# Kernel optimization log

Measured on AMD Instinct MI355X. Metric: run time of the kernel, lower is better.

The kernel has to match this reference:

```python
import jax, jax.numpy as jnp
import numpy as np

N = 100000
E = 1600000
C = 128
SIM_THRESH = 0.2
DEG_THRESH = 3.0


def setup_inputs() -> dict:
    key = jax.random.key(0)
    ks = jax.random.split(key, 10)
    g = 0.1  # glorot-ish scale for prompt params
    x = jax.random.normal(ks[0], (N, C), jnp.float32)
    edge_index = jax.random.randint(ks[1], (2, E), 0, N)
    prompt_sim = jax.random.normal(ks[2], (1, C), jnp.float32) * g
    prompt_degree = jax.random.normal(ks[3], (1, C), jnp.float32) * g
    prompt_other = jax.random.normal(ks[4], (1, C), jnp.float32) * g
    readout_token = jax.random.normal(ks[5], (1, 1, C), jnp.float32) * g
    in_proj_w = jax.random.normal(ks[6], (3 * C, C), jnp.float32) / np.sqrt(C)
    in_proj_b = jnp.zeros((3 * C,), jnp.float32)
    out_proj_w = jax.random.normal(ks[7], (C, C), jnp.float32) / np.sqrt(C)
    out_proj_b = jnp.zeros((C,), jnp.float32)
    return {"x": x, "prompt_sim": prompt_sim, "prompt_degree": prompt_degree,
            "prompt_other": prompt_other, "readout_token": readout_token,
            "in_proj_w": in_proj_w, "in_proj_b": in_proj_b,
            "out_proj_w": out_proj_w, "out_proj_b": out_proj_b,
            "edge_index": edge_index}


def _forward(x, prompt_sim, prompt_degree, prompt_other, readout_token,
             in_proj_w, in_proj_b, out_proj_w, out_proj_b, edge_index):
    n = x.shape[0]
    row, col = edge_index[0], edge_index[1]

    # per-edge cosine similarity, scatter-added to destination nodes
    x_norm = x / jnp.sqrt(jnp.sum(x * x, axis=1, keepdims=True))  # [N,C]
    e = jnp.sum(x_norm[row] * x_norm[col], axis=1)                # [E]
    c = jax.ops.segment_sum(e, col, num_segments=n)               # [N]
    deg = jax.ops.segment_sum(jnp.ones_like(e), col, num_segments=n)  # [N]
    csim = jax.lax.stop_gradient(c / deg)                         # nan for deg==0 -> mask False

    sim_mask = csim <= SIM_THRESH                                 # [N] bool
    deg_mask = jax.lax.stop_gradient(deg) <= DEG_THRESH
    other_mask = ~(sim_mask | deg_mask)

    neg1 = jnp.float32(-1.0)
    slot0 = jnp.where(sim_mask[:, None], prompt_sim, neg1)        # [N,C]
    slot1 = jnp.where(deg_mask[:, None], prompt_degree, neg1)
    slot2 = jnp.where(other_mask[:, None], prompt_other, neg1)
    rec = jnp.stack([slot0, slot1, slot2], axis=1)                # [N,3,C]
    ro = jnp.broadcast_to(readout_token, (n, 1, x.shape[1]))
    rec = jnp.concatenate([ro, rec], axis=1)                      # [N,4,C]

    # key_padding_mask: True where slot entirely -1 (unfilled)
    kpm = jnp.all(rec == neg1, axis=-1)                           # [N,4]

    # single-head MHA over the 4 prompt slots per node
    qkv = rec @ in_proj_w.T + in_proj_b                           # [N,4,3C]
    q, k, v = jnp.split(qkv, 3, axis=-1)
    scale = 1.0 / np.sqrt(rec.shape[-1])
    scores = jnp.einsum('nqc,nkc->nqk', q, k) * scale             # [N,4,4]
    scores = jnp.where(kpm[:, None, :], -jnp.inf, scores)
    attn = jax.nn.softmax(scores, axis=-1)
    out = jnp.einsum('nqk,nkc->nqc', attn, v)
    out = out @ out_proj_w.T + out_proj_b                         # [N,4,C]

    final = out[:, 0, :]                                          # readout slot
    return x + final


def reference(x, prompt_sim, prompt_degree, prompt_other, readout_token,
              in_proj_w, in_proj_b, out_proj_w, out_proj_b, edge_index):
    return _forward(x, prompt_sim, prompt_degree, prompt_other, readout_token,
                    in_proj_w, in_proj_b, out_proj_w, out_proj_b, edge_index)
```

## Files before the change

### kernel.cpp

```cpp
#include <hip/hip_runtime.h>
#include <hip/hip_bf16.h>
#include <math.h>

#define C 128
#define SIM_THRESH 0.2f
#define DEG_THRESH 3.0f

#define FIX_SCALE 16777216.0f
#define FIX_INV   5.9604644775390625e-8f

typedef float floatx2 __attribute__((ext_vector_type(2)));

__device__ __forceinline__ void gemv_body(int blk,
        const float* __restrict__ ps, const float* __restrict__ pd,
        const float* __restrict__ po, const float* __restrict__ ro,
        const float* __restrict__ W,  const float* __restrict__ b,
        const float* __restrict__ Wo,
        float* __restrict__ qb, float* __restrict__ kb, float* __restrict__ vpb) {
    int g  = blk >> 2;
    int qt = blk & 3;
    int gi = threadIdx.x >> 3;
    int li = threadIdx.x & 7;

    int bi = (g == 0) ? 0 : (g <= 4 ? g - 1 : g - 5);
    const float* src = (bi == 0) ? ro : (bi == 1 ? ps : (bi == 2 ? pd : po));
    float4 s4[4];
    #pragma unroll
    for (int k = 0; k < 4; ++k) s4[k] = ((const float4*)src)[8 * k + li];

    if (g <= 4) {
        int rowoff = (g == 0) ? 0 : C;
        int t = qt * 32 + gi;
        const float* Wr = W + (size_t)(rowoff + t) * C;
        float p = 0.0f;
        #pragma unroll
        for (int k = 0; k < 4; ++k) {
            float4 w4 = ((const float4*)Wr)[8 * k + li];
            p += w4.x * s4[k].x + w4.y * s4[k].y + w4.z * s4[k].z + w4.w * s4[k].w;
        }
        p += __shfl_xor(p, 1, 64);
        p += __shfl_xor(p, 2, 64);
        p += __shfl_xor(p, 4, 64);
        if (li == 0) {
            if (g == 0) qb[t] = p + b[t];
            else        kb[(g - 1) * C + t] = p + b[C + t];
        }
    } else {
        __shared__ float vbuf[C];
        #pragma unroll
        for (int j = 0; j < 4; ++j) {
            int t = gi + 32 * j;
            const float* Wr = W + (size_t)(2 * C + t) * C;
            float p = 0.0f;
            #pragma unroll
            for (int k = 0; k < 4; ++k) {
                float4 w4 = ((const float4*)Wr)[8 * k + li];
                p += w4.x * s4[k].x + w4.y * s4[k].y + w4.z * s4[k].z + w4.w * s4[k].w;
            }
            p += __shfl_xor(p, 1, 64);
            p += __shfl_xor(p, 2, 64);
            p += __shfl_xor(p, 4, 64);
            if (li == 0) vbuf[t] = p + b[2 * C + t];
        }
        __syncthreads();
        float4 v4[4];
        #pragma unroll
        for (int k = 0; k < 4; ++k) v4[k] = ((const float4*)vbuf)[8 * k + li];
        int t = qt * 32 + gi;
        const float* Wr = Wo + (size_t)t * C;
        float p = 0.0f;
        #pragma unroll
        for (int k = 0; k < 4; ++k) {
            float4 w4 = ((const float4*)Wr)[8 * k + li];
            p += w4.x * v4[k].x + w4.y * v4[k].y + w4.z * v4[k].z + w4.w * v4[k].w;
        }
        p += __shfl_xor(p, 1, 64);
        p += __shfl_xor(p, 2, 64);
        p += __shfl_xor(p, 4, 64);
        if (li == 0) vpb[(g - 5) * C + t] = p;
    }
}

__device__ __forceinline__ void combine_body(
        const float* __restrict__ qb, const float* __restrict__ kb,
        const float* __restrict__ vpb, const float* __restrict__ bo,
        float* __restrict__ finals) {
    __shared__ float attn_s[4][4];
    int wv = threadIdx.x >> 6;
    int lane = threadIdx.x & 63;
    if (wv == 0) {
        float2 qv = ((const float2*)qb)[lane];
        float d[4];
        #pragma unroll
        for (int bI = 0; bI < 4; ++bI) {
            float2 kv = ((const float2*)(kb + bI * C))[lane];
            float p = qv.x * kv.x + qv.y * kv.y;
            #pragma unroll
            for (int off = 32; off; off >>= 1) p += __shfl_xor(p, off, 64);
            d[bI] = p;
        }
        if (lane == 0) {
            const float scale = 0.08838834764831845f;
            for (int combo = 0; combo < 4; ++combo) {
                bool sim = (combo & 1), degm = (combo & 2), other = !(sim || degm);
                bool act[4] = { true, sim, degm, other };
                float m = -INFINITY;
                #pragma unroll
                for (int j = 0; j < 4; ++j) if (act[j]) m = fmaxf(m, d[j] * scale);
                float w[4], den = 0.0f;
                #pragma unroll
                for (int j = 0; j < 4; ++j) {
                    w[j] = act[j] ? expf(d[j] * scale - m) : 0.0f;
                    den += w[j];
                }
                #pragma unroll
                for (int j = 0; j < 4; ++j) attn_s[combo][j] = w[j] / den;
            }
        }
    }
    __syncthreads();
    int t = threadIdx.x;
    if (t < C) {
        for (int combo = 0; combo < 4; ++combo) {
            float f = bo[t];
            #pragma unroll
            for (int j = 0; j < 4; ++j) f += attn_s[combo][j] * vpb[j * C + t];
            finals[combo * C + t] = f;
        }
    }
}

__global__ void prep_kernel(const float* __restrict__ x, unsigned int* __restrict__ xn,
                            unsigned long long* __restrict__ packed,
                            const float* __restrict__ ps, const float* __restrict__ pd,
                            const float* __restrict__ po, const float* __restrict__ ro,
                            const float* __restrict__ W,  const float* __restrict__ b,
                            const float* __restrict__ Wo,
                            float* __restrict__ qb, float* __restrict__ kb,
                            float* __restrict__ vpb, int N) {
    if (blockIdx.x < 36) {
        gemv_body(blockIdx.x, ps, pd, po, ro, W, b, Wo, qb, kb, vpb);
        return;
    }
    int grp = threadIdx.x >> 5;
    int l   = threadIdx.x & 31;
    int row = (blockIdx.x - 36) * 8 + grp;
    if (row >= N) return;
    float4 a = ((const float4*)(x + (size_t)row * C))[l];
    float s = a.x * a.x + a.y * a.y + a.z * a.z + a.w * a.w;
    #pragma unroll
    for (int off = 16; off; off >>= 1) s += __shfl_xor(s, off, 64);
    float r = rsqrtf(s);
    int u = __builtin_amdgcn_cvt_pk_fp8_f32(a.x * r, a.y * r, 0, false);
    u     = __builtin_amdgcn_cvt_pk_fp8_f32(a.z * r, a.w * r, u, true);
    xn[(size_t)row * 32 + l] = (unsigned int)u;
    if (l == 0) packed[row] = 0ULL;
}

__global__ void edge_kernel_fp8(const uint4* __restrict__ xn4, const int* __restrict__ ei,
                                unsigned long long* __restrict__ packed, int E,
                                const float* __restrict__ qb, const float* __restrict__ kb,
                                const float* __restrict__ vpb, const float* __restrict__ bo,
                                float* __restrict__ finals) {
    if (blockIdx.x == 0) {
        combine_body(qb, kb, vpb, bo, finals);
        return;
    }
    int gid  = (blockIdx.x - 1) * blockDim.x + threadIdx.x;
    int edge = gid >> 3;
    int lane = threadIdx.x & 7;
    if (edge >= E) return;
    int r = ei[edge];
    int c = ei[E + edge];
    uint4 a = xn4[(size_t)r * 8 + lane];
    uint4 b = xn4[(size_t)c * 8 + lane];
    float dot = 0.0f;
    #pragma unroll
    for (int k = 0; k < 4; ++k) {
        int ua = (int)(&a.x)[k], ub = (int)(&b.x)[k];
        floatx2 a0 = __builtin_amdgcn_cvt_pk_f32_fp8(ua, false);
        floatx2 a1 = __builtin_amdgcn_cvt_pk_f32_fp8(ua, true);
        floatx2 b0 = __builtin_amdgcn_cvt_pk_f32_fp8(ub, false);
        floatx2 b1 = __builtin_amdgcn_cvt_pk_f32_fp8(ub, true);
        dot += a0.x * b0.x + a0.y * b0.y + a1.x * b1.x + a1.y * b1.y;
    }
    #pragma unroll
    for (int off = 4; off; off >>= 1) dot += __shfl_xor(dot, off, 64);
    if (lane == 0) {
        long long fx = (long long)llrintf(dot * FIX_SCALE);
        atomicAdd(&packed[c], (1ULL << 40) + (unsigned long long)fx);
    }
}

__global__ void gemv_kernel(const float* __restrict__ ps, const float* __restrict__ pd,
                            const float* __restrict__ po, const float* __restrict__ ro,
                            const float* __restrict__ W,  const float* __restrict__ b,
                            const float* __restrict__ Wo,
                            float* __restrict__ qb, float* __restrict__ kb,
                            float* __restrict__ vpb) {
    gemv_body(blockIdx.x, ps, pd, po, ro, W, b, Wo, qb, kb, vpb);
}

__global__ void norm_kernel(const float* __restrict__ x, float* __restrict__ rnorm,
                            unsigned long long* __restrict__ packed, int N) {
    int row  = (blockIdx.x * blockDim.x + threadIdx.x) >> 6;
    int lane = threadIdx.x & 63;
    if (row >= N) return;
    float2 a = ((const float2*)(x + (size_t)row * C))[lane];
    float s = a.x * a.x + a.y * a.y;
    #pragma unroll
    for (int off = 32; off; off >>= 1) s += __shfl_xor(s, off, 64);
    if (lane == 0) { rnorm[row] = rsqrtf(s); packed[row] = 0ULL; }
}

__global__ void edge_kernel_f32(const float* __restrict__ x, const int* __restrict__ ei,
                                const float* __restrict__ rnorm,
                                unsigned long long* __restrict__ packed, int E,
                                const float* __restrict__ qb, const float* __restrict__ kb,
                                const float* __restrict__ vpb, const float* __restrict__ bo,
                                float* __restrict__ finals) {
    if (blockIdx.x == 0) {
        combine_body(qb, kb, vpb, bo, finals);
        return;
    }
    int gid  = (blockIdx.x - 1) * blockDim.x + threadIdx.x;
    int edge = gid >> 5;
    int lane = threadIdx.x & 31;
    if (edge >= E) return;
    int r = ei[edge];
    int c = ei[E + edge];
    float4 a = ((const float4*)(x + (size_t)r * C))[lane];
    float4 b = ((const float4*)(x + (size_t)c * C))[lane];
    float dot = a.x * b.x + a.y * b.y + a.z * b.z + a.w * b.w;
    #pragma unroll
    for (int off = 16; off; off >>= 1) dot += __shfl_xor(dot, off, 64);
    if (lane == 0) {
        float e = dot * rnorm[r] * rnorm[c];
        long long fx = (long long)llrintf(e * FIX_SCALE);
        atomicAdd(&packed[c], (1ULL << 40) + (unsigned long long)fx);
    }
}

__global__ void apply_kernel(const float* __restrict__ x,
                             const unsigned long long* __restrict__ packed,
                             const float* __restrict__ finals,
                             float* __restrict__ out, int N) {
    size_t i = (size_t)blockIdx.x * blockDim.x + threadIdx.x;
    size_t total = (size_t)N * (C / 4);
    if (i >= total) return;
    int row = (int)(i >> 5);
    unsigned long long v = packed[row];
    long long d_ll = (long long)((v + (1ULL << 39)) >> 40);
    long long s_ll = (long long)(v - ((unsigned long long)d_ll << 40));
    float d  = (float)d_ll;
    float cs = (float)s_ll * FIX_INV;
    bool sim  = (d_ll > 0) && ((cs / d) <= SIM_THRESH);
    bool degm = d <= DEG_THRESH;
    int combo = (sim ? 1 : 0) | (degm ? 2 : 0);
    float4 xv = ((const float4*)x)[i];
    float4 fv = ((const float4*)finals)[(size_t)combo * 32 + (i & 31)];
    float4 o  = { xv.x + fv.x, xv.y + fv.y, xv.z + fv.z, xv.w + fv.w };
    ((float4*)out)[i] = o;
}

extern "C" void kernel_launch(void* const* d_in, const int* in_sizes, int n_in,
                              void* d_out, int out_size, void* d_ws, size_t ws_size,
                              hipStream_t stream) {
    const float* x             = (const float*)d_in[0];
    const float* prompt_sim    = (const float*)d_in[1];
    const float* prompt_degree = (const float*)d_in[2];
    const float* prompt_other  = (const float*)d_in[3];
    const float* readout       = (const float*)d_in[4];
    const float* in_proj_w     = (const float*)d_in[5];
    const float* in_proj_b     = (const float*)d_in[6];
    const float* out_proj_w    = (const float*)d_in[7];
    const float* out_proj_b    = (const float*)d_in[8];
    const int*   edge_index    = (const int*)d_in[9];

    const int N = in_sizes[0] / C;
    const int E = in_sizes[9] / 2;
    float* out = (float*)d_out;

    unsigned long long* packed = (unsigned long long*)d_ws;
    float* finals = (float*)(packed + N);
    float* qb     = finals + 4 * C;
    float* kb     = qb + C;
    float* vpb    = kb + 4 * C;
    float* rnorm  = vpb + 4 * C;
    size_t head_bytes = ((size_t)N * 8 + (size_t)(13 * C + N) * sizeof(float) + 255) & ~(size_t)255;
    unsigned int* xn = (unsigned int*)((char*)d_ws + head_bytes);
    size_t need = head_bytes + (size_t)N * C;
    bool fp8_path = (ws_size >= need);

    if (fp8_path) {
        int nRowBlocks = (N + 7) / 8;
        prep_kernel<<<nRowBlocks + 36, 256, 0, stream>>>(
            x, xn, packed, prompt_sim, prompt_degree, prompt_other, readout,
            in_proj_w, in_proj_b, out_proj_w, qb, kb, vpb, N);
        {
            long long lanes = (long long)E * 8;
            int blocks = 1 + (int)((lanes + 255) / 256);
            edge_kernel_fp8<<<blocks, 256, 0, stream>>>((const uint4*)xn, edge_index, packed, E,
                                                        qb, kb, vpb, out_proj_b, finals);
        }
    } else {
        gemv_kernel<<<36, 256, 0, stream>>>(prompt_sim, prompt_degree, prompt_other, readout,
                                            in_proj_w, in_proj_b, out_proj_w, qb, kb, vpb);
        {
            int blocks = (N * 64 + 255) / 256;
            norm_kernel<<<blocks, 256, 0, stream>>>(x, rnorm, packed, N);
        }
        {
            long long lanes = (long long)E * 32;
            int blocks = 1 + (int)((lanes + 255) / 256);
            edge_kernel_f32<<<blocks, 256, 0, stream>>>(x, edge_index, rnorm, packed, E,
                                                        qb, kb, vpb, out_proj_b, finals);
        }
    }

    {
        long long work = (long long)N * (C / 4);
        int blocks = (int)((work + 255) / 256);
        apply_kernel<<<blocks, 256, 0, stream>>>(x, packed, finals, out, N);
    }
}
```

Baseline: 207.6 us.

## Fuse prep, edge and apply stages into one cooperative persistent kernel

Replaces the three separate launches (prep, edge, apply) with a single cooperative kernel on a fixed 1024-block grid. Grid-stride loops cover each phase, and grid.sync() separates them. The aim is to remove per-launch overhead and inter-kernel gaps. In exchange it adds two grid-wide barriers, a fixed grid size that may underuse the device or limit occupancy, a device attribute query on every call, and removal of the fp32 fallback path.

```diff
diff --git a/kernel.cpp b/kernel.cpp
--- a/kernel.cpp
+++ b/kernel.cpp
@@ -1,6 +1,9 @@
 #include <hip/hip_runtime.h>
+#include <hip/hip_cooperative_groups.h>
 #include <hip/hip_bf16.h>
 #include <math.h>
+
+namespace cg = cooperative_groups;
 
 #define C 128
 #define SIM_THRESH 0.2f
@@ -10,6 +13,15 @@
 #define FIX_INV   5.9604644775390625e-8f
 
 typedef float floatx2 __attribute__((ext_vector_type(2)));
+
+struct Params {
+    const float *x, *ps, *pd, *po, *ro, *W, *b, *Wo, *bo;
+    const int *ei;
+    unsigned int *xn;
+    unsigned long long *packed;
+    float *qb, *kb, *vpb, *finals, *out;
+    int N, E;
+};
 
 __device__ __forceinline__ void gemv_body(int blk,
         const float* __restrict__ ps, const float* __restrict__ pd,
@@ -130,6 +142,81 @@
     }
 }
 
+__global__ __launch_bounds__(256, 4) void fused_kernel(Params P) {
+    cg::grid_group grid = cg::this_grid();
+    const int bid = blockIdx.x;
+    const int tid = threadIdx.x;
+    const int nb  = gridDim.x;
+
+    if (bid < 36)
+        gemv_body(bid, P.ps, P.pd, P.po, P.ro, P.W, P.b, P.Wo, P.qb, P.kb, P.vpb);
+    {
+        int grp = tid >> 5, l = tid & 31;
+        for (int row = bid * 8 + grp; row < P.N; row += nb * 8) {
+            float4 a = ((const float4*)(P.x + (size_t)row * C))[l];
+            float s = a.x * a.x + a.y * a.y + a.z * a.z + a.w * a.w;
+            #pragma unroll
+            for (int off = 16; off; off >>= 1) s += __shfl_xor(s, off, 64);
+            float r = rsqrtf(s);
+            int u = __builtin_amdgcn_cvt_pk_fp8_f32(a.x * r, a.y * r, 0, false);
+            u     = __builtin_amdgcn_cvt_pk_fp8_f32(a.z * r, a.w * r, u, true);
+            P.xn[(size_t)row * 32 + l] = (unsigned int)u;
+            if (l == 0) P.packed[row] = 0ULL;
+        }
+    }
+    grid.sync();
+
+    if (bid == 0) combine_body(P.qb, P.kb, P.vpb, P.bo, P.finals);
+    {
+        const uint4* xn4 = (const uint4*)P.xn;
+        int lane = tid & 7;
+        int step = (nb * 256) >> 3;
+        for (int e = (bid * 256 + tid) >> 3; e < P.E; e += step) {
+            int r = P.ei[e];
+            int c = P.ei[P.E + e];
+            uint4 a = xn4[(size_t)r * 8 + lane];
+            uint4 b = xn4[(size_t)c * 8 + lane];
+            float dot = 0.0f;
+            #pragma unroll
+            for (int k = 0; k < 4; ++k) {
+                int ua = (int)(&a.x)[k], ub = (int)(&b.x)[k];
+                floatx2 a0 = __builtin_amdgcn_cvt_pk_f32_fp8(ua, false);
+                floatx2 a1 = __builtin_amdgcn_cvt_pk_f32_fp8(ua, true);
+                floatx2 b0 = __builtin_amdgcn_cvt_pk_f32_fp8(ub, false);
+                floatx2 b1 = __builtin_amdgcn_cvt_pk_f32_fp8(ub, true);
+                dot += a0.x * b0.x + a0.y * b0.y + a1.x * b1.x + a1.y * b1.y;
+            }
+            dot += __shfl_xor(dot, 1, 64);
+            dot += __shfl_xor(dot, 2, 64);
+            dot += __shfl_xor(dot, 4, 64);
+            if (lane == 0) {
+                long long fx = (long long)llrintf(dot * FIX_SCALE);
+                atomicAdd(&P.packed[c], (1ULL << 40) + (unsigned long long)fx);
+            }
+        }
+    }
+    grid.sync();
+
+    {
+        size_t total = (size_t)P.N * 32;
+        for (size_t i = (size_t)bid * 256 + tid; i < total; i += (size_t)nb * 256) {
+            int row = (int)(i >> 5);
+            unsigned long long v = P.packed[row];
+            long long d_ll = (long long)((v + (1ULL << 39)) >> 40);
+            long long s_ll = (long long)(v - ((unsigned long long)d_ll << 40));
+            float d  = (float)d_ll;
+            float cs = (float)s_ll * FIX_INV;
+            bool sim  = (d_ll > 0) && ((cs / d) <= SIM_THRESH);
+            bool degm = d <= DEG_THRESH;
+            int combo = (sim ? 1 : 0) | (degm ? 2 : 0);
+            float4 xv = ((const float4*)P.x)[i];
+            float4 fv = ((const float4*)P.finals)[(size_t)combo * 32 + (i & 31)];
+            float4 o  = { xv.x + fv.x, xv.y + fv.y, xv.z + fv.z, xv.w + fv.w };
+            ((float4*)P.out)[i] = o;
+        }
+    }
+}
+
 __global__ void prep_kernel(const float* __restrict__ x, unsigned int* __restrict__ xn,
                             unsigned long long* __restrict__ packed,
                             const float* __restrict__ ps, const float* __restrict__ pd,
@@ -188,55 +275,6 @@
     for (int off = 4; off; off >>= 1) dot += __shfl_xor(dot, off, 64);
     if (lane == 0) {
         long long fx = (long long)llrintf(dot * FIX_SCALE);
-        atomicAdd(&packed[c], (1ULL << 40) + (unsigned long long)fx);
-    }
-}
-
-__global__ void gemv_kernel(const float* __restrict__ ps, const float* __restrict__ pd,
-                            const float* __restrict__ po, const float* __restrict__ ro,
-                            const float* __restrict__ W,  const float* __restrict__ b,
-                            const float* __restrict__ Wo,
-                            float* __restrict__ qb, float* __restrict__ kb,
-                            float* __restrict__ vpb) {
-    gemv_body(blockIdx.x, ps, pd, po, ro, W, b, Wo, qb, kb, vpb);
-}
-
-__global__ void norm_kernel(const float* __restrict__ x, float* __restrict__ rnorm,
-                            unsigned long long* __restrict__ packed, int N) {
-    int row  = (blockIdx.x * blockDim.x + threadIdx.x) >> 6;
-    int lane = threadIdx.x & 63;
-    if (row >= N) return;
-    float2 a = ((const float2*)(x + (size_t)row * C))[lane];
-    float s = a.x * a.x + a.y * a.y;
-    #pragma unroll
-    for (int off = 32; off; off >>= 1) s += __shfl_xor(s, off, 64);
-    if (lane == 0) { rnorm[row] = rsqrtf(s); packed[row] = 0ULL; }
-}
-
-__global__ void edge_kernel_f32(const float* __restrict__ x, const int* __restrict__ ei,
-                                const float* __restrict__ rnorm,
-                                unsigned long long* __restrict__ packed, int E,
-                                const float* __restrict__ qb, const float* __restrict__ kb,
-                                const float* __restrict__ vpb, const float* __restrict__ bo,
-                                float* __restrict__ finals) {
-    if (blockIdx.x == 0) {
-        combine_body(qb, kb, vpb, bo, finals);
-        return;
-    }
-    int gid  = (blockIdx.x - 1) * blockDim.x + threadIdx.x;
-    int edge = gid >> 5;
-    int lane = threadIdx.x & 31;
-    if (edge >= E) return;
-    int r = ei[edge];
-    int c = ei[E + edge];
-    float4 a = ((const float4*)(x + (size_t)r * C))[lane];
-    float4 b = ((const float4*)(x + (size_t)c * C))[lane];
-    float dot = a.x * b.x + a.y * b.y + a.z * b.z + a.w * b.w;
-    #pragma unroll
-    for (int off = 16; off; off >>= 1) dot += __shfl_xor(dot, off, 64);
-    if (lane == 0) {
-        float e = dot * rnorm[r] * rnorm[c];
-        long long fx = (long long)llrintf(e * FIX_SCALE);
         atomicAdd(&packed[c], (1ULL << 40) + (unsigned long long)fx);
     }
 }
@@ -266,61 +304,53 @@
 extern "C" void kernel_launch(void* const* d_in, const int* in_sizes, int n_in,
                               void* d_out, int out_size, void* d_ws, size_t ws_size,
                               hipStream_t stream) {
-    const float* x             = (const float*)d_in[0];
-    const float* prompt_sim    = (const float*)d_in[1];
-    const float* prompt_degree = (const float*)d_in[2];
-    const float* prompt_other  = (const float*)d_in[3];
-    const float* readout       = (const float*)d_in[4];
-    const float* in_proj_w     = (const float*)d_in[5];
-    const float* in_proj_b     = (const float*)d_in[6];
-    const float* out_proj_w    = (const float*)d_in[7];
-    const float* out_proj_b    = (const float*)d_in[8];
-    const int*   edge_index    = (const int*)d_in[9];
-
-    const int N = in_sizes[0] / C;
-    const int E = in_sizes[9] / 2;
-    float* out = (float*)d_out;
-
-    unsigned long long* packed = (unsigned long long*)d_ws;
-    float* finals = (float*)(packed + N);
-    float* qb     = finals + 4 * C;
-    float* kb     = qb + C;
-    float* vpb    = kb + 4 * C;
-    float* rnorm  = vpb + 4 * C;
-    size_t head_bytes = ((size_t)N * 8 + (size_t)(13 * C + N) * sizeof(float) + 255) & ~(size_t)255;
-    unsigned int* xn = (unsigned int*)((char*)d_ws + head_bytes);
-    size_t need = head_bytes + (size_t)N * C;
-    bool fp8_path = (ws_size >= need);
-
-    if (fp8_path) {
-        int nRowBlocks = (N + 7) / 8;
-        prep_kernel<<<nRowBlocks + 36, 256, 0, stream>>>(
-            x, xn, packed, prompt_sim, prompt_degree, prompt_other, readout,
-            in_proj_w, in_proj_b, out_proj_w, qb, kb, vpb, N);
+    Params P;
+    P.x  = (const float*)d_in[0];
+    P.ps = (const float*)d_in[1];
+    P.pd = (const float*)d_in[2];
+    P.po = (const float*)d_in[3];
+    P.ro = (const float*)d_in[4];
+    P.W  = (const float*)d_in[5];
+    P.b  = (const float*)d_in[6];
+    P.Wo = (const float*)d_in[7];
+    P.bo = (const float*)d_in[8];
+    P.ei = (const int*)d_in[9];
+    P.N  = in_sizes[0] / C;
+    P.E  = in_sizes[9] / 2;
+    P.out = (float*)d_out;
+
+    P.packed = (unsigned long long*)d_ws;
+    P.finals = (float*)(P.packed + P.N);
+    P.qb     = P.finals + 4 * C;
+    P.kb     = P.qb + C;
+    P.vpb    = P.kb + 4 * C;
+    size_t head_bytes = ((size_t)P.N * 8 + (size_t)(13 * C) * sizeof(float) + 255) & ~(size_t)255;
+    P.xn = (unsigned int*)((char*)d_ws + head_bytes);
+
+    int coop = 0;
+    hipDeviceGetAttribute(&coop, hipDeviceAttributeCooperativeLaunch, 0);
+
+    if (coop) {
+        void* args[] = { (void*)&P };
+        hipLaunchCooperativeKernel((const void*)fused_kernel, dim3(1024), dim3(256),
+                                   args, 0, stream);
+    } else {
         {
-            long long lanes = (long long)E * 8;
+            int nRowBlocks = (P.N + 7) / 8;
+            prep_kernel<<<nRowBlocks + 36, 256, 0, stream>>>(
+                P.x, P.xn, P.packed, P.ps, P.pd, P.po, P.ro,
+                P.W, P.b, P.Wo, P.qb, P.kb, P.vpb, P.N);
+        }
+        {
+            long long lanes = (long long)P.E * 8;
             int blocks = 1 + (int)((lanes + 255) / 256);
-            edge_kernel_fp8<<<blocks, 256, 0, stream>>>((const uint4*)xn, edge_index, packed, E,
-                                                        qb, kb, vpb, out_proj_b, finals);
-        }
-    } else {
-        gemv_kernel<<<36, 256, 0, stream>>>(prompt_sim, prompt_degree, prompt_other, readout,
-                                            in_proj_w, in_proj_b, out_proj_w, qb, kb, vpb);
+            edge_kernel_fp8<<<blocks, 256, 0, stream>>>((const uint4*)P.xn, P.ei, P.packed, P.E,
+                                                        P.qb, P.kb, P.vpb, P.bo, P.finals);
+        }
         {
-            int blocks = (N * 64 + 255) / 256;
-            norm_kernel<<<blocks, 256, 0, stream>>>(x, rnorm, packed, N);
-        }
-        {
-            long long lanes = (long long)E * 32;
-            int blocks = 1 + (int)((lanes + 255) / 256);
-            edge_kernel_f32<<<blocks, 256, 0, stream>>>(x, edge_index, rnorm, packed, E,
-                                                        qb, kb, vpb, out_proj_b, finals);
-        }
-    }
-
-    {
-        long long work = (long long)N * (C / 4);
-        int blocks = (int)((work + 255) / 256);
-        apply_kernel<<<blocks, 256, 0, stream>>>(x, packed, finals, out, N);
-    }
-}
+            long long work = (long long)P.N * (C / 4);
+            int blocks = (int)((work + 255) / 256);
+            apply_kernel<<<blocks, 256, 0, stream>>>(P.x, P.packed, P.finals, P.out, P.N);
+        }
+    }
+}
```

Result: slower. 472.0 us (+127.4%).
